# Kernel tuning notes

Hardware: AMD Instinct MI355X
Metric: run time of the kernel (lower is better)

The kernel has to match this reference:

```python
import jax, jax.numpy as jnp
import numpy as np
from functools import lru_cache


@lru_cache(maxsize=None)
def _mw_basis(L):
    """Fully-normalized associated Legendre basis on MW-style theta grid.

    Returns (Pfull, w):
      Pfull: (L, 2L-1, L) float32, Pfull[l, L-1+m, t] = Nbar_lm * P_l^m(cos theta_t)
             (zero for |m| > l), with Y_lm = Pfull * exp(i m phi).
      w:     (L,) float32 quadrature weights sin(theta)*dtheta*dphi.
    """
    t = np.arange(L)
    theta = np.pi * (2 * t + 1) / (2 * L - 1)  # MW theta samples
    ct, st = np.cos(theta), np.sin(theta)
    P = np.zeros((L, L, L))
    P[0, 0] = np.full(L, np.sqrt(1.0 / (4.0 * np.pi)))
    for m in range(1, L):
        P[m, m] = -np.sqrt((2.0 * m + 1.0) / (2.0 * m)) * st * P[m - 1, m - 1]
    for m in range(L - 1):
        P[m + 1, m] = np.sqrt(2.0 * m + 3.0) * ct * P[m, m]
    for m in range(L):
        for l in range(m + 2, L):
            a = np.sqrt((4.0 * l * l - 1.0) / (l * l - m * m))
            b = np.sqrt(((2.0 * l + 1.0) * (l - 1 - m) * (l - 1 + m)) / ((2.0 * l - 3.0) * (l * l - m * m)))
            P[l, m] = a * ct * P[l - 1, m] - b * P[l - 2, m]
    Pfull = np.zeros((L, 2 * L - 1, L), dtype=np.float32)
    for m in range(L):
        Pfull[:, L - 1 + m, :] = P[:, m, :]
        if m > 0:
            Pfull[:, L - 1 - m, :] = ((-1.0) ** m) * P[:, m, :]
    dang = 2.0 * np.pi / (2 * L - 1)  # theta and phi spacing
    w = (st * dang * dang).astype(np.float32)
    return jnp.asarray(Pfull), jnp.asarray(w)


def sht_forward(x):
    """x: (L, 2L-1, C) real -> flm: (L, 2L-1, C) complex, m indexed -(L-1)..(L-1)."""
    L = x.shape[0]
    P, w = _mw_basis(L)
    F = jnp.fft.fft(x.astype(jnp.complex64), axis=1)           # k = 0..2L-2
    F = jnp.concatenate([F[:, L:, :], F[:, :L, :]], axis=1)     # reorder to m = -(L-1)..L-1
    # flm = sum_t w_t Nbar P_l^m(theta_t) * Fm(theta_t)
    return jnp.einsum('lmt,tmc->lmc', P * w[None, None, :], F)


def sht_inverse(flm):
    """flm: (L, 2L-1, C) complex -> f: (L, 2L-1, C) complex on MW grid."""
    L = flm.shape[0]
    P, _ = _mw_basis(L)
    G = jnp.einsum('lmc,lmt->tmc', flm, P)                      # (theta, m, C)
    G = jnp.concatenate([G[:, L - 1:, :], G[:, :L - 1, :]], axis=1)  # m order -> fft k order
    return jnp.fft.ifft(G, axis=1) * (2 * L - 1)


def zero_pad_flm(flm, L_out):
    L_in = flm.shape[0]
    p = L_out - L_in
    return jnp.pad(flm, ((0, p), (p, p), (0, 0)))


L_IN = 256
L_FREQ = 128
L_OUT = 256
C_IN = 32
C_OUT = 32
T_DIM = 256


def setup_inputs() -> dict:
    key = jax.random.key(0)
    ks = jax.random.split(key, 8)
    return {
        'x': jax.random.normal(ks[0], (L_IN, 2 * L_IN - 1, C_IN), jnp.float32),
        't_emb': jax.random.normal(ks[1], (T_DIM,), jnp.float32),
        'weight_real': 0.02 * jax.random.normal(ks[2], (L_FREQ, C_IN, C_OUT), jnp.float32),
        'weight_imag': 0.02 * jax.random.normal(ks[3], (L_FREQ, C_IN, C_OUT), jnp.float32),
        'w_tr': jax.random.normal(ks[4], (T_DIM, L_FREQ), jnp.float32) / np.sqrt(T_DIM),
        'b_tr': jnp.zeros((L_FREQ,), jnp.float32),
        'w_ti': jax.random.normal(ks[5], (T_DIM, L_FREQ), jnp.float32) / np.sqrt(T_DIM),
        'b_ti': jnp.zeros((L_FREQ,), jnp.float32),
    }


def reference(x, t_emb, weight_real, weight_imag, w_tr, b_tr, w_ti, b_ti):
    # forward SHT over all channels at once
    flm = sht_forward(x)                                       # (L_in, 2L_in-1, C_in) complex64
    # bilinear resize of the spectrum to the used bandlimit (real/imag separately)
    tgt = (L_FREQ, 2 * L_FREQ - 1, flm.shape[2])
    flm = (jax.image.resize(jnp.real(flm), tgt, 'bilinear')
           + 1j * jax.image.resize(jnp.imag(flm), tgt, 'bilinear'))
    # time-modulated per-degree complex spectral weights
    t_cplx = (t_emb @ w_tr + b_tr) + 1j * (t_emb @ w_ti + b_ti)   # (L_freq,)
    weight = t_cplx[:, None, None] * (weight_real + 1j * weight_imag)  # (L_freq, C_in, C_out)
    flm = jnp.einsum('lmi,lio->lmo', flm, weight)
    # zero pad to output bandlimit and inverse SHT
    flm = zero_pad_flm(flm, L_OUT)                             # (L_out, 2L_out-1, C_out)
    x_out = jnp.real(sht_inverse(flm))
    return x_out
```

## Files before the change

kernel.cpp:

```cpp
#include <hip/hip_runtime.h>
#include <math.h>

#define PI_D 3.14159265358979323846

typedef short v8s __attribute__((ext_vector_type(8)));
typedef float v4f __attribute__((ext_vector_type(4)));

constexpr size_t OFF_PA   = 0;
constexpr size_t OFF_PT   = 8388608;
constexpr size_t OFF_SFRE = 12582912;
constexpr size_t OFF_SFIM = 14680064;
constexpr size_t OFF_FRE  = 16777216;
constexpr size_t OFF_FIM  = 18874368;
constexpr size_t OFF_CRE  = 20971520;
constexpr size_t OFF_CIM  = 22016000;
constexpr size_t OFF_AF   = 23060480;
constexpr size_t OFF_AI   = 23191552;
constexpr size_t OFF_WQ   = 23322624;
constexpr size_t OFF_TC   = 23322880;
constexpr size_t OFF_WLW  = 23323136;
constexpr size_t OFF_WLI  = 23323648;
constexpr size_t OFF_WMW  = 23324160;
constexpr size_t OFF_WMI  = 23325696;
constexpr size_t OFF_GRE  = OFF_FRE;
constexpr size_t OFF_GIM  = OFF_FIM;

__device__ __forceinline__ short f2bf(float f) {
  unsigned u = __float_as_uint(f);
  unsigned r = (u + 0x7FFFu + ((u >> 16) & 1u)) >> 16;
  return (short)r;
}


__device__ void phase_prep(const float* t_emb, const float* w_tr, const float* b_tr,
                           const float* w_ti, const float* b_ti, float* ws, int g0, int tid) {
  if (g0 < 2048) {
    int g = g0 * 256 + tid;
    bool inv = (g >= 262144);
    int gid = inv ? g - 262144 : g;
    int j = gid & 7, lane = (gid >> 3) & 63, ks = (gid >> 9) & 15, mt = gid >> 13;
    int m = mt * 16 + (lane & 15);
    int k = ks * 32 + ((lane >> 4) << 3) + j;
    float v = 0.f;
    if (!inv) {
      if (k < 511) {
        int mm = (m < 256) ? m : m - 256;
        int kk = (mm * k) % 511;
        float ang = (float)(2.0 * PI_D / 511.0) * (float)kk;
        float s, c; __sincosf(ang, &s, &c);
        v = (m < 256) ? c : -s;
      }
      ((short*)(ws + OFF_AF))[gid] = f2bf(v);
    } else {
      if (m < 511 && k < 510) {
        int jj = (k < 255) ? k : k - 255;
        int jm = jj - 127;
        int kk = ((jm * m) % 511 + 511) % 511;
        float ang = (float)(2.0 * PI_D / 511.0) * (float)kk;
        float s, c; __sincosf(ang, &s, &c);
        v = (k < 255) ? c : -s;
      }
      ((short*)(ws + OFF_AI))[gid] = f2bf(v);
    }
    return;
  }
  if (tid < 256) {
    double theta = PI_D * (2.0 * tid + 1.0) / 511.0;
    double dang = 2.0 * PI_D / 511.0;
    ws[OFF_WQ + tid] = (float)(sin(theta) * dang * dang);
  }
  {
    int h = tid >> 7, o = tid & 127;
    const float* W = h ? w_ti : w_tr;
    float s = h ? b_ti[o] : b_tr[o];
    for (int T = 0; T < 256; ++T) s += t_emb[T] * W[T * 128 + o];
    ws[OFF_TC + h * 128 + o] = s;
  }
  if (tid < 128) {
    double sf = 2.0 * tid + 0.5;
    double wv[4]; int iv[4]; double wsum = 0.0;
    for (int a = 0; a < 4; ++a) {
      int t = 2 * tid - 1 + a;
      double r = 1.0 - fabs(sf - (double)t) * 0.5;
      bool valid = (t >= 0 && t < 256 && r > 0.0);
      wv[a] = valid ? r : 0.0; iv[a] = valid ? t : 0;
      wsum += wv[a];
    }
    for (int a = 0; a < 4; ++a) {
      ws[OFF_WLW + tid * 4 + a] = (float)(wv[a] / wsum);
      ((int*)(ws + OFF_WLI))[tid * 4 + a] = iv[a];
    }
  }
  if (tid < 255) {
    double inv2 = 511.0 / 255.0;
    double sf = (tid + 0.5) * inv2 - 0.5;
    int t0 = (int)floor(sf) - 2;
    double wv[6]; int iv[6]; double wsum = 0.0;
    for (int b = 0; b < 6; ++b) {
      int t = t0 + b;
      double r = 1.0 - fabs(sf - (double)t) * (255.0 / 511.0);
      bool valid = (t >= 0 && t < 511 && r > 0.0);
      wv[b] = valid ? r : 0.0; iv[b] = valid ? t : 0;
      wsum += wv[b];
    }
    for (int b = 0; b < 6; ++b) {
      ws[OFF_WMW + tid * 6 + b] = (float)(wv[b] / wsum);
      ((int*)(ws + OFF_WMI))[tid * 6 + b] = iv[b];
    }
  }
}

__device__ void phase_legendre(float* ws, char* smem, int m, int t) {
  double* cA = (double*)smem;
  double* cB = cA + 256;
  double* cS = cB + 256;
  short* tile = (short*)(smem + 6144);
  short* tileT = (short*)(smem + 6144 + 8960);
  {
    int l = t;
    if (l >= 1) cS[l] = -sqrt((2.0 * l + 1.0) / (2.0 * l));
    if (l >= m + 2) {
      double ll = l, mm = m;
      double den = ll * ll - mm * mm;
      cA[l] = sqrt((4.0 * ll * ll - 1.0) / den);
      cB[l] = sqrt((2.0 * ll + 1.0) * (ll - 1.0 - mm) * (ll - 1.0 + mm) /
                   ((2.0 * ll - 3.0) * den));
    }
  }
  __syncthreads();
  bool wantPT = (m < 128);
  short* PAp = (short*)(ws + OFF_PA) + (size_t)m * 65536;
  short* PTp = (short*)(ws + OFF_PT) + (size_t)m * 65536;
  double theta = PI_D * (2.0 * t + 1.0) / 511.0;
  double ct = cos(theta), st = sin(theta);
  double p0 = sqrt(1.0 / (4.0 * PI_D));
  for (int k = 1; k <= m; ++k) p0 *= cS[k] * st;
  double pm1 = 0.0, pcur = 0.0;
  for (int lt = 0; lt < 16; ++lt) {
    for (int li = 0; li < 16; ++li) {
      int l = lt * 16 + li;
      float v;
      if (l < m) v = 0.f;
      else if (l == m) { pcur = p0; v = (float)pcur; }
      else if (l == m + 1) { pm1 = pcur; pcur = sqrt(2.0 * m + 3.0) * ct * pm1; v = (float)pcur; }
      else { double p2 = cA[l] * ct * pcur - cB[l] * pm1; pm1 = pcur; pcur = p2; v = (float)p2; }
      short bv = f2bf(v);
      tile[li * 280 + t] = bv;
      if (wantPT) tileT[t * 34 + li] = bv;
    }
    __syncthreads();
#pragma unroll
    for (int pass = 0; pass < 2; ++pass) {
      int ch = pass * 256 + t;
      int li = ch & 15, T0 = ch >> 4;
      size_t dst = (size_t)lt * 4096 + (size_t)(T0 >> 2) * 512 + (size_t)((T0 & 3) * 16 + li) * 8;
      *(v8s*)(PAp + dst) = *(const v8s*)(tile + li * 280 + T0 * 8);
    }
    if (wantPT) {
#pragma unroll
      for (int pass = 0; pass < 2; ++pass) {
        int ch = pass * 256 + t;
        int tt = ch >> 1, li0 = (ch & 1) * 8;
        size_t dst = (size_t)(tt >> 4) * 4096 + (size_t)(lt >> 1) * 512 +
                     (size_t)(((lt & 1) * 2 + (li0 >> 3)) * 16 + (tt & 15)) * 8;
        const int* src = (const int*)(tileT + tt * 34 + li0);
        int* d = (int*)(PTp + dst);
        d[0] = src[0]; d[1] = src[1]; d[2] = src[2]; d[3] = src[3];
      }
    }
    __syncthreads();
  }
}

__device__ void phase_gemm_f(const float* x, float* ws, short* lds, int uid, int tid) {
  int nt = uid & 1, mh = (uid >> 1) & 1, t = uid >> 2;
  int wave = tid >> 6, lane = tid & 63;
  const v8s* A = (const v8s*)(ws + OFF_AF);
  float wq = ws[OFF_WQ + t];
  const float* row = x + (size_t)t * 511 * 32 + nt * 16;
  int cl = lane & 15, quad = lane >> 4;
  int mtB = mh * 16 + wave * 4;
  int ck = tid >> 4, cc = tid & 15;
  v4f acc[4];
#pragma unroll
  for (int i = 0; i < 4; ++i) acc[i] = (v4f){0.f, 0.f, 0.f, 0.f};
  v8s a_cur[4], a_nxt[4];
#pragma unroll
  for (int i = 0; i < 4; ++i) a_cur[i] = A[(size_t)((mtB + i) * 16 + 0) * 64 + lane];
  {
    float p0 = wq * row[(size_t)ck * 32 + cc];
    float p1 = wq * row[(size_t)(ck + 16) * 32 + cc];
    lds[cc * 40 + ck] = f2bf(p0);
    lds[cc * 40 + ck + 16] = f2bf(p1);
  }
  __syncthreads();
  for (int ks = 0; ks < 16; ++ks) {
    float n0 = 0.f, n1 = 0.f;
    if (ks < 15) {
      int ph0 = (ks + 1) * 32 + ck, ph1 = ph0 + 16;
      n0 = (ph0 < 511) ? wq * row[(size_t)ph0 * 32 + cc] : 0.f;
      n1 = (ph1 < 511) ? wq * row[(size_t)ph1 * 32 + cc] : 0.f;
#pragma unroll
      for (int i = 0; i < 4; ++i)
        a_nxt[i] = A[(size_t)((mtB + i) * 16 + ks + 1) * 64 + lane];
    }
    v8s b = *(const v8s*)(lds + (ks & 1) * 640 + cl * 40 + quad * 8);
#pragma unroll
    for (int i = 0; i < 4; ++i)
      acc[i] = __builtin_amdgcn_mfma_f32_16x16x32_bf16(a_cur[i], b, acc[i], 0, 0, 0);
    if (ks < 15) {
      short* nb = lds + ((ks + 1) & 1) * 640;
      nb[cc * 40 + ck] = f2bf(n0);
      nb[cc * 40 + ck + 16] = f2bf(n1);
#pragma unroll
      for (int i = 0; i < 4; ++i) a_cur[i] = a_nxt[i];
      __syncthreads();
    }
  }
  int cn = nt * 16 + cl;
#pragma unroll
  for (int i = 0; i < 4; ++i) {
    int mt = mtB + i;
#pragma unroll
    for (int r = 0; r < 4; ++r) {
      int mp = mt * 16 + quad * 4 + r;
      float v = acc[i][r];
      if (mp < 256) ws[OFF_FRE + ((size_t)mp * 256 + t) * 32 + cn] = v;
      else          ws[OFF_FIM + ((size_t)(mp - 256) * 256 + t) * 32 + cn] = v;
    }
  }
}

__device__ void phase_legfwd(float* ws, short* lds, int uid, int tid) {
  int m = uid >> 2, q = uid & 3;
  int lane = tid & 63;
  int cl = lane & 15, quad = lane >> 4;
  if (q * 64 + 63 < m) {
    int mt = q * 4 + (tid >> 6);
#pragma unroll
    for (int n = 0; n < 4; ++n) {
      int cp = n * 16 + cl;
      float* dst = ws + ((cp >= 32) ? OFF_SFIM : OFF_SFRE) + (size_t)m * 8192 + (cp & 31);
#pragma unroll
      for (int r = 0; r < 4; ++r) {
        int l = mt * 16 + quad * 4 + r;
        dst[(size_t)l * 32] = 0.f;
      }
    }
    return;
  }
  int mt = q * 4 + (tid >> 6);
  bool sk = (mt * 16 + 15) < m;
  const v8s* A = (const v8s*)(ws + OFF_PA) + (size_t)m * 8192;
  int half = (tid >> 5) & 1, c = tid & 31, tb = tid >> 6;
  const float* srcb = ws + (half ? OFF_FIM : OFF_FRE) + (size_t)m * 8192 + c;
  short* myrow = lds;
  int ldsw = (half * 32 + c) * 40 + tb;
  v4f acc[4];
#pragma unroll
  for (int n = 0; n < 4; ++n) acc[n] = (v4f){0.f, 0.f, 0.f, 0.f};
  v8s a_cur = A[(size_t)mt * 512 + lane];
  v8s a_nxt;
  {
    float pv[8];
#pragma unroll
    for (int pass = 0; pass < 8; ++pass)
      pv[pass] = srcb[(size_t)(pass * 4 + tb) * 32];
#pragma unroll
    for (int pass = 0; pass < 8; ++pass)
      myrow[ldsw + pass * 4] = f2bf(pv[pass]);
  }
  __syncthreads();
  for (int ks = 0; ks < 8; ++ks) {
    float pn[8];
    if (ks < 7) {
#pragma unroll
      for (int pass = 0; pass < 8; ++pass)
        pn[pass] = srcb[(size_t)((ks + 1) * 32 + pass * 4 + tb) * 32];
      a_nxt = A[(size_t)mt * 512 + (ks + 1) * 64 + lane];
    }
    const short* cur = lds + (ks & 1) * 2560;
    if (!sk) {
#pragma unroll
      for (int n = 0; n < 4; ++n) {
        v8s b = *(const v8s*)(cur + (n * 16 + cl) * 40 + quad * 8);
        acc[n] = __builtin_amdgcn_mfma_f32_16x16x32_bf16(a_cur, b, acc[n], 0, 0, 0);
      }
    }
    if (ks < 7) {
      short* nb = lds + ((ks + 1) & 1) * 2560;
#pragma unroll
      for (int pass = 0; pass < 8; ++pass)
        nb[ldsw + pass * 4] = f2bf(pn[pass]);
      a_cur = a_nxt;
      __syncthreads();
    }
  }
#pragma unroll
  for (int n = 0; n < 4; ++n) {
    int cp = n * 16 + cl;
    float* dst = ws + ((cp >= 32) ? OFF_SFIM : OFF_SFRE) + (size_t)m * 8192 + (cp & 31);
#pragma unroll
    for (int r = 0; r < 4; ++r) {
      int l = mt * 16 + quad * 4 + r;
      dst[(size_t)l * 32] = sk ? 0.f : acc[n][r];
    }
  }
}

__device__ void phase_conv(const float* w_real, const float* w_imag, float* ws, char* smem,
                           int uid, int tid) {
  int l = uid >> 3, jq8 = uid & 7;
  int jl = tid >> 5, o = tid & 31;
  float* wr = (float*)smem;
  float* wi = wr + 32 * 36;
  float* fr = wi + 32 * 36;
  float* fi = fr + 8 * 32;
  {
    int oo = tid >> 3, i4 = (tid & 7) * 4;
    float tcr = ws[OFF_TC + l], tci = ws[OFF_TC + 128 + l];
#pragma unroll
    for (int q = 0; q < 4; ++q) {
      int i = i4 + q;
      float a = w_real[(size_t)l * 1024 + i * 32 + oo];
      float b = w_imag[(size_t)l * 1024 + i * 32 + oo];
      wr[oo * 36 + i] = tcr * a - tci * b;
      wi[oo * 36 + i] = tcr * b + tci * a;
    }
  }
  const float* SFRE = ws + OFF_SFRE;
  const float* SFIM = ws + OFF_SFIM;
  const float* WMW = ws + OFF_WMW;
  const int* WMI = (const int*)(ws + OFF_WMI);
  float wl[4]; int liv[4];
#pragma unroll
  for (int a = 0; a < 4; ++a) {
    wl[a] = ws[OFF_WLW + l * 4 + a];
    liv[a] = ((const int*)(ws + OFF_WLI))[l * 4 + a];
  }
  for (int ji = 0; ji < 4; ++ji) {
    int j = jq8 * 32 + ji * 8 + jl;
    int jp = (j < 255) ? j : 254;
    float accr = 0.f, acci = 0.f;
    for (int b = 0; b < 6; ++b) {
      float wm = WMW[jp * 6 + b];
      int jm = WMI[jp * 6 + b];
      bool mneg = (jm < 255);
      int mm = mneg ? (255 - jm) : (jm - 255);
      float fre_f = (mneg && (mm & 1)) ? -1.f : 1.f;
      float fim_f = mneg ? -fre_f : 1.f;
#pragma unroll
      for (int a = 0; a < 4; ++a) {
        float w = wm * wl[a];
        size_t base = ((size_t)mm * 256 + liv[a]) * 32 + o;
        accr = fmaf(w * fre_f, SFRE[base], accr);
        acci = fmaf(w * fim_f, SFIM[base], acci);
      }
    }
    __syncthreads();
    fr[jl * 32 + o] = accr;
    fi[jl * 32 + o] = acci;
    __syncthreads();
    float sr = 0.f, si = 0.f;
#pragma unroll
    for (int i0 = 0; i0 < 32; i0 += 4) {
      float4 f_r = *(const float4*)(fr + jl * 32 + i0);
      float4 f_i = *(const float4*)(fi + jl * 32 + i0);
      float4 w_r = *(const float4*)(wr + o * 36 + i0);
      float4 w_i = *(const float4*)(wi + o * 36 + i0);
      sr += f_r.x * w_r.x - f_i.x * w_i.x;  si += f_r.x * w_i.x + f_i.x * w_r.x;
      sr += f_r.y * w_r.y - f_i.y * w_i.y;  si += f_r.y * w_i.y + f_i.y * w_r.y;
      sr += f_r.z * w_r.z - f_i.z * w_i.z;  si += f_r.z * w_i.z + f_i.z * w_r.z;
      sr += f_r.w * w_r.w - f_i.w * w_i.w;  si += f_r.w * w_i.w + f_i.w * w_r.w;
    }
    if (j < 255) {
      float s = (j < 127 && ((127 - j) & 1)) ? -1.f : 1.f;
      ws[OFF_CRE + ((size_t)j * 128 + l) * 32 + o] = s * sr;
      ws[OFF_CIM + ((size_t)j * 128 + l) * 32 + o] = s * si;
    }
  }
}

__device__ void phase_linv(float* ws, int uid, int tid) {
  int j = uid >> 2;
  int d = j - 127; int mm = (d < 0) ? -d : d;
  int mt = (uid & 3) * 4 + (tid >> 6), lane = tid & 63;
  const v8s* A = (const v8s*)(ws + OFF_PT) + (size_t)mm * 8192;
  int cl = lane & 15, lB = (lane >> 4) << 3;
  int quad = lane >> 4;
  v4f acc[4];
#pragma unroll
  for (int n = 0; n < 4; ++n) acc[n] = (v4f){0.f, 0.f, 0.f, 0.f};
  int ks0 = mm >> 5;
  const float* Cb[4];
#pragma unroll
  for (int n = 0; n < 4; ++n) {
    int cp = n * 16 + cl;
    Cb[n] = ws + (cp < 32 ? OFF_CRE : OFF_CIM) + ((size_t)j * 128 + lB) * 32 + (cp & 31);
  }
  float bv[4][8];
  v8s a_cur = A[(size_t)mt * 512 + ks0 * 64 + lane];
#pragma unroll
  for (int n = 0; n < 4; ++n)
#pragma unroll
    for (int j8 = 0; j8 < 8; ++j8) bv[n][j8] = Cb[n][(size_t)(ks0 * 32 + j8) * 32];
  for (int ks = ks0; ks < 4; ++ks) {
    float bn[4][8];
    v8s a_nxt;
    if (ks < 3) {
#pragma unroll
      for (int n = 0; n < 4; ++n)
#pragma unroll
        for (int j8 = 0; j8 < 8; ++j8) bn[n][j8] = Cb[n][(size_t)((ks + 1) * 32 + j8) * 32];
      a_nxt = A[(size_t)mt * 512 + (ks + 1) * 64 + lane];
    }
#pragma unroll
    for (int n = 0; n < 4; ++n) {
      v8s b;
#pragma unroll
      for (int j8 = 0; j8 < 8; ++j8) b[j8] = f2bf(bv[n][j8]);
      acc[n] = __builtin_amdgcn_mfma_f32_16x16x32_bf16(a_cur, b, acc[n], 0, 0, 0);
    }
    if (ks < 3) {
#pragma unroll
      for (int n = 0; n < 4; ++n)
#pragma unroll
        for (int j8 = 0; j8 < 8; ++j8) bv[n][j8] = bn[n][j8];
      a_cur = a_nxt;
    }
  }
#pragma unroll
  for (int n = 0; n < 4; ++n) {
    int cp = n * 16 + cl;
    float* dst = ws + ((cp >= 32) ? OFF_GIM : OFF_GRE) + (size_t)(cp & 31);
#pragma unroll
    for (int r = 0; r < 4; ++r) {
      int t = mt * 16 + quad * 4 + r;
      dst[((size_t)t * 255 + j) * 32] = acc[n][r];
    }
  }
}

__device__ void phase_gemm_i(const float* ws, float* out, short* lds, int uid, int tid) {
  int nt = uid & 1, mh = (uid >> 1) & 1, t = uid >> 2;
  int wave = tid >> 6, lane = tid & 63;
  const v8s* A = (const v8s*)(ws + OFF_AI);
  const float* GRE = ws + OFF_GRE;
  const float* GIM = ws + OFF_GIM;
  int cl = lane & 15, quad = lane >> 4;
  int mtB = mh * 16 + wave * 4;
  int cn = nt * 16 + cl;
  int ck = tid >> 4, cc = tid & 15;
  int ccg = nt * 16 + cc;
  v4f acc[4];
#pragma unroll
  for (int i = 0; i < 4; ++i) acc[i] = (v4f){0.f, 0.f, 0.f, 0.f};
  v8s a_cur[4], a_nxt[4];
#pragma unroll
  for (int i = 0; i < 4; ++i) a_cur[i] = A[(size_t)((mtB + i) * 16 + 0) * 64 + lane];
  {
    float p0 = GRE[((size_t)t * 255 + ck) * 32 + ccg];
    float p1 = GRE[((size_t)t * 255 + ck + 16) * 32 + ccg];
    lds[cc * 40 + ck] = f2bf(p0);
    lds[cc * 40 + ck + 16] = f2bf(p1);
  }
  __syncthreads();
  for (int ks = 0; ks < 16; ++ks) {
    float n0 = 0.f, n1 = 0.f;
    if (ks < 15) {
      int k0 = (ks + 1) * 32 + ck, k1 = k0 + 16;
      if (k0 < 255)      n0 = GRE[((size_t)t * 255 + k0) * 32 + ccg];
      else if (k0 < 510) n0 = GIM[((size_t)t * 255 + (k0 - 255)) * 32 + ccg];
      if (k1 < 255)      n1 = GRE[((size_t)t * 255 + k1) * 32 + ccg];
      else if (k1 < 510) n1 = GIM[((size_t)t * 255 + (k1 - 255)) * 32 + ccg];
#pragma unroll
      for (int i = 0; i < 4; ++i)
        a_nxt[i] = A[(size_t)((mtB + i) * 16 + ks + 1) * 64 + lane];
    }
    v8s b = *(const v8s*)(lds + (ks & 1) * 640 + cl * 40 + quad * 8);
#pragma unroll
    for (int i = 0; i < 4; ++i)
      acc[i] = __builtin_amdgcn_mfma_f32_16x16x32_bf16(a_cur[i], b, acc[i], 0, 0, 0);
    if (ks < 15) {
      short* nb = lds + ((ks + 1) & 1) * 640;
      nb[cc * 40 + ck] = f2bf(n0);
      nb[cc * 40 + ck + 16] = f2bf(n1);
#pragma unroll
      for (int i = 0; i < 4; ++i) a_cur[i] = a_nxt[i];
      __syncthreads();
    }
  }
#pragma unroll
  for (int i = 0; i < 4; ++i) {
    int mt = mtB + i;
#pragma unroll
    for (int r = 0; r < 4; ++r) {
      int phi = mt * 16 + quad * 4 + r;
      if (phi < 511) out[((size_t)t * 511 + phi) * 32 + cn] = acc[i][r];
    }
  }
}

__global__ __launch_bounds__(256) void k_prepleg(const float* t_emb, const float* w_tr,
                                                 const float* b_tr, const float* w_ti,
                                                 const float* b_ti, float* ws) {
  __shared__ __align__(16) char smem[32768];
  int bid = blockIdx.x;
  if (bid < 256) phase_legendre(ws, smem, bid, threadIdx.x);
  else phase_prep(t_emb, w_tr, b_tr, w_ti, b_ti, ws, bid - 256, threadIdx.x);
}
__global__ __launch_bounds__(256) void kw_gemm_f(const float* x, float* ws) {
  __shared__ __align__(16) short lds[2 * 640];
  phase_gemm_f(x, ws, lds, blockIdx.x, threadIdx.x);
}
__global__ __launch_bounds__(256) void kw_legfwd(float* ws) {
  __shared__ __align__(16) short lds[2 * 2560];
  phase_legfwd(ws, lds, blockIdx.x, threadIdx.x);
}
__global__ __launch_bounds__(256) void kw_conv(const float* w_real, const float* w_imag, float* ws) {
  __shared__ __align__(16) char smem[11264];
  phase_conv(w_real, w_imag, ws, smem, blockIdx.x, threadIdx.x);
}
__global__ __launch_bounds__(256) void kw_linv(float* ws) {
  phase_linv(ws, blockIdx.x, threadIdx.x);
}
__global__ __launch_bounds__(256) void kw_gemm_i(const float* ws, float* out) {
  __shared__ __align__(16) short lds[2 * 640];
  phase_gemm_i(ws, out, lds, blockIdx.x, threadIdx.x);
}

extern "C" void kernel_launch(void* const* d_in, const int* in_sizes, int n_in,
                              void* d_out, int out_size, void* d_ws, size_t ws_size,
                              hipStream_t stream) {
  const float* x = (const float*)d_in[0];
  const float* t_emb = (const float*)d_in[1];
  const float* w_real = (const float*)d_in[2];
  const float* w_imag = (const float*)d_in[3];
  const float* w_tr = (const float*)d_in[4];
  const float* b_tr = (const float*)d_in[5];
  const float* w_ti = (const float*)d_in[6];
  const float* b_ti = (const float*)d_in[7];
  float* ws = (float*)d_ws;
  float* out = (float*)d_out;
  (void)in_sizes; (void)n_in; (void)out_size; (void)ws_size;

  hipLaunchKernelGGL(k_prepleg, dim3(2305), dim3(256), 0, stream,
                     t_emb, w_tr, b_tr, w_ti, b_ti, ws);
  hipLaunchKernelGGL(kw_gemm_f, dim3(1024), dim3(256), 0, stream, x, ws);
  hipLaunchKernelGGL(kw_legfwd, dim3(1024), dim3(256), 0, stream, ws);
  hipLaunchKernelGGL(kw_conv, dim3(1024), dim3(256), 0, stream, w_real, w_imag, ws);
  hipLaunchKernelGGL(kw_linv, dim3(1020), dim3(256), 0, stream, ws);
  hipLaunchKernelGGL(kw_gemm_i, dim3(1024), dim3(256), 0, stream, ws, out);
}
```

Before: 188.3 us.

## Stage full B operand in LDS upfront and skip zero Legendre tile stores

Three GEMM phases (forward DFT GEMM, forward Legendre, inverse DFT GEMM) now load the whole B operand into LDS once, using packed 8-wide bf16 stores, and no longer double-buffer it. This removes the per-iteration barriers and the interleaved global loads inside the k-loop. The forward Legendre phase also skips A-tile loads for fully-zero m tiles. The Legendre table builder skips writing tiles that lie entirely below l=m, assuming those regions are never read or are already zero. The cost is a much larger LDS footprint per block (about 16–33KB), which may lower occupancy, and the global loads are no longer overlapped with the MFMAs.

```diff
diff --git a/kernel.cpp b/kernel.cpp
--- a/kernel.cpp
+++ b/kernel.cpp
@@ -149,14 +149,16 @@
       if (wantPT) tileT[t * 34 + li] = bv;
     }
     __syncthreads();
-#pragma unroll
-    for (int pass = 0; pass < 2; ++pass) {
-      int ch = pass * 256 + t;
-      int li = ch & 15, T0 = ch >> 4;
-      size_t dst = (size_t)lt * 4096 + (size_t)(T0 >> 2) * 512 + (size_t)((T0 & 3) * 16 + li) * 8;
-      *(v8s*)(PAp + dst) = *(const v8s*)(tile + li * 280 + T0 * 8);
-    }
-    if (wantPT) {
+    if (lt * 16 + 15 >= m) {
+#pragma unroll
+      for (int pass = 0; pass < 2; ++pass) {
+        int ch = pass * 256 + t;
+        int li = ch & 15, T0 = ch >> 4;
+        size_t dst = (size_t)lt * 4096 + (size_t)(T0 >> 2) * 512 + (size_t)((T0 & 3) * 16 + li) * 8;
+        *(v8s*)(PAp + dst) = *(const v8s*)(tile + li * 280 + T0 * 8);
+      }
+    }
+    if (wantPT && ((lt >> 1) >= (m >> 5))) {
 #pragma unroll
       for (int pass = 0; pass < 2; ++pass) {
         int ch = pass * 256 + t;
@@ -180,41 +182,43 @@
   const float* row = x + (size_t)t * 511 * 32 + nt * 16;
   int cl = lane & 15, quad = lane >> 4;
   int mtB = mh * 16 + wave * 4;
-  int ck = tid >> 4, cc = tid & 15;
+  {
+    int c = tid & 15, kc = tid >> 4;
+#pragma unroll
+    for (int i = 0; i < 4; ++i) {
+      int k0 = (kc + 16 * i) * 8;
+      float pv[8];
+#pragma unroll
+      for (int j = 0; j < 8; ++j) {
+        int k = k0 + j;
+        pv[j] = (k < 511) ? wq * row[(size_t)k * 32 + c] : 0.f;
+      }
+      v8s tmp;
+#pragma unroll
+      for (int j = 0; j < 8; ++j) tmp[j] = f2bf(pv[j]);
+      *(v8s*)(lds + c * 520 + k0) = tmp;
+    }
+  }
   v4f acc[4];
 #pragma unroll
   for (int i = 0; i < 4; ++i) acc[i] = (v4f){0.f, 0.f, 0.f, 0.f};
   v8s a_cur[4], a_nxt[4];
 #pragma unroll
   for (int i = 0; i < 4; ++i) a_cur[i] = A[(size_t)((mtB + i) * 16 + 0) * 64 + lane];
-  {
-    float p0 = wq * row[(size_t)ck * 32 + cc];
-    float p1 = wq * row[(size_t)(ck + 16) * 32 + cc];
-    lds[cc * 40 + ck] = f2bf(p0);
-    lds[cc * 40 + ck + 16] = f2bf(p1);
-  }
   __syncthreads();
   for (int ks = 0; ks < 16; ++ks) {
-    float n0 = 0.f, n1 = 0.f;
     if (ks < 15) {
-      int ph0 = (ks + 1) * 32 + ck, ph1 = ph0 + 16;
-      n0 = (ph0 < 511) ? wq * row[(size_t)ph0 * 32 + cc] : 0.f;
-      n1 = (ph1 < 511) ? wq * row[(size_t)ph1 * 32 + cc] : 0.f;
 #pragma unroll
       for (int i = 0; i < 4; ++i)
         a_nxt[i] = A[(size_t)((mtB + i) * 16 + ks + 1) * 64 + lane];
     }
-    v8s b = *(const v8s*)(lds + (ks & 1) * 640 + cl * 40 + quad * 8);
+    v8s b = *(const v8s*)(lds + cl * 520 + ks * 32 + quad * 8);
 #pragma unroll
     for (int i = 0; i < 4; ++i)
       acc[i] = __builtin_amdgcn_mfma_f32_16x16x32_bf16(a_cur[i], b, acc[i], 0, 0, 0);
     if (ks < 15) {
-      short* nb = lds + ((ks + 1) & 1) * 640;
-      nb[cc * 40 + ck] = f2bf(n0);
-      nb[cc * 40 + ck + 16] = f2bf(n1);
 #pragma unroll
       for (int i = 0; i < 4; ++i) a_cur[i] = a_nxt[i];
-      __syncthreads();
     }
   }
   int cn = nt * 16 + cl;
@@ -252,48 +256,37 @@
   int mt = q * 4 + (tid >> 6);
   bool sk = (mt * 16 + 15) < m;
   const v8s* A = (const v8s*)(ws + OFF_PA) + (size_t)m * 8192;
-  int half = (tid >> 5) & 1, c = tid & 31, tb = tid >> 6;
-  const float* srcb = ws + (half ? OFF_FIM : OFF_FRE) + (size_t)m * 8192 + c;
-  short* myrow = lds;
-  int ldsw = (half * 32 + c) * 40 + tb;
+  {
+    int half = (tid >> 5) & 1, c = tid & 31, tb = tid >> 6;
+    const float* srcb = ws + (half ? OFF_FIM : OFF_FRE) + (size_t)m * 8192 + c;
+    int ldsrow = (half * 32 + c) * 264;
+#pragma unroll
+    for (int p = 0; p < 8; ++p) {
+      int t0 = (p * 4 + tb) * 8;
+      float pv[8];
+#pragma unroll
+      for (int j = 0; j < 8; ++j) pv[j] = srcb[(size_t)(t0 + j) * 32];
+      v8s tmp;
+#pragma unroll
+      for (int j = 0; j < 8; ++j) tmp[j] = f2bf(pv[j]);
+      *(v8s*)(lds + ldsrow + t0) = tmp;
+    }
+  }
   v4f acc[4];
 #pragma unroll
   for (int n = 0; n < 4; ++n) acc[n] = (v4f){0.f, 0.f, 0.f, 0.f};
-  v8s a_cur = A[(size_t)mt * 512 + lane];
-  v8s a_nxt;
-  {
-    float pv[8];
-#pragma unroll
-    for (int pass = 0; pass < 8; ++pass)
-      pv[pass] = srcb[(size_t)(pass * 4 + tb) * 32];
-#pragma unroll
-    for (int pass = 0; pass < 8; ++pass)
-      myrow[ldsw + pass * 4] = f2bf(pv[pass]);
-  }
+  v8s a_cur, a_nxt;
+  if (!sk) a_cur = A[(size_t)mt * 512 + lane];
   __syncthreads();
   for (int ks = 0; ks < 8; ++ks) {
-    float pn[8];
-    if (ks < 7) {
-#pragma unroll
-      for (int pass = 0; pass < 8; ++pass)
-        pn[pass] = srcb[(size_t)((ks + 1) * 32 + pass * 4 + tb) * 32];
-      a_nxt = A[(size_t)mt * 512 + (ks + 1) * 64 + lane];
-    }
-    const short* cur = lds + (ks & 1) * 2560;
+    if (!sk && ks < 7) a_nxt = A[(size_t)mt * 512 + (ks + 1) * 64 + lane];
     if (!sk) {
 #pragma unroll
       for (int n = 0; n < 4; ++n) {
-        v8s b = *(const v8s*)(cur + (n * 16 + cl) * 40 + quad * 8);
+        v8s b = *(const v8s*)(lds + (n * 16 + cl) * 264 + ks * 32 + quad * 8);
         acc[n] = __builtin_amdgcn_mfma_f32_16x16x32_bf16(a_cur, b, acc[n], 0, 0, 0);
       }
-    }
-    if (ks < 7) {
-      short* nb = lds + ((ks + 1) & 1) * 2560;
-#pragma unroll
-      for (int pass = 0; pass < 8; ++pass)
-        nb[ldsw + pass * 4] = f2bf(pn[pass]);
-      a_cur = a_nxt;
-      __syncthreads();
+      if (ks < 7) a_cur = a_nxt;
     }
   }
 #pragma unroll
@@ -450,44 +443,47 @@
   int cl = lane & 15, quad = lane >> 4;
   int mtB = mh * 16 + wave * 4;
   int cn = nt * 16 + cl;
-  int ck = tid >> 4, cc = tid & 15;
-  int ccg = nt * 16 + cc;
+  {
+    int c = tid & 15, kc = tid >> 4;
+    int ccg = nt * 16 + c;
+#pragma unroll
+    for (int i = 0; i < 4; ++i) {
+      int k0 = (kc + 16 * i) * 8;
+      float pv[8];
+#pragma unroll
+      for (int j = 0; j < 8; ++j) {
+        int k = k0 + j;
+        float v = 0.f;
+        if (k < 255)      v = GRE[((size_t)t * 255 + k) * 32 + ccg];
+        else if (k < 510) v = GIM[((size_t)t * 255 + (k - 255)) * 32 + ccg];
+        pv[j] = v;
+      }
+      v8s tmp;
+#pragma unroll
+      for (int j = 0; j < 8; ++j) tmp[j] = f2bf(pv[j]);
+      *(v8s*)(lds + c * 520 + k0) = tmp;
+    }
+  }
   v4f acc[4];
 #pragma unroll
   for (int i = 0; i < 4; ++i) acc[i] = (v4f){0.f, 0.f, 0.f, 0.f};
   v8s a_cur[4], a_nxt[4];
 #pragma unroll
   for (int i = 0; i < 4; ++i) a_cur[i] = A[(size_t)((mtB + i) * 16 + 0) * 64 + lane];
-  {
-    float p0 = GRE[((size_t)t * 255 + ck) * 32 + ccg];
-    float p1 = GRE[((size_t)t * 255 + ck + 16) * 32 + ccg];
-    lds[cc * 40 + ck] = f2bf(p0);
-    lds[cc * 40 + ck + 16] = f2bf(p1);
-  }
   __syncthreads();
   for (int ks = 0; ks < 16; ++ks) {
-    float n0 = 0.f, n1 = 0.f;
     if (ks < 15) {
-      int k0 = (ks + 1) * 32 + ck, k1 = k0 + 16;
-      if (k0 < 255)      n0 = GRE[((size_t)t * 255 + k0) * 32 + ccg];
-      else if (k0 < 510) n0 = GIM[((size_t)t * 255 + (k0 - 255)) * 32 + ccg];
-      if (k1 < 255)      n1 = GRE[((size_t)t * 255 + k1) * 32 + ccg];
-      else if (k1 < 510) n1 = GIM[((size_t)t * 255 + (k1 - 255)) * 32 + ccg];
 #pragma unroll
       for (int i = 0; i < 4; ++i)
         a_nxt[i] = A[(size_t)((mtB + i) * 16 + ks + 1) * 64 + lane];
     }
-    v8s b = *(const v8s*)(lds + (ks & 1) * 640 + cl * 40 + quad * 8);
+    v8s b = *(const v8s*)(lds + cl * 520 + ks * 32 + quad * 8);
 #pragma unroll
     for (int i = 0; i < 4; ++i)
       acc[i] = __builtin_amdgcn_mfma_f32_16x16x32_bf16(a_cur[i], b, acc[i], 0, 0, 0);
     if (ks < 15) {
-      short* nb = lds + ((ks + 1) & 1) * 640;
-      nb[cc * 40 + ck] = f2bf(n0);
-      nb[cc * 40 + ck + 16] = f2bf(n1);
 #pragma unroll
       for (int i = 0; i < 4; ++i) a_cur[i] = a_nxt[i];
-      __syncthreads();
     }
   }
 #pragma unroll
@@ -510,11 +506,11 @@
   else phase_prep(t_emb, w_tr, b_tr, w_ti, b_ti, ws, bid - 256, threadIdx.x);
 }
 __global__ __launch_bounds__(256) void kw_gemm_f(const float* x, float* ws) {
-  __shared__ __align__(16) short lds[2 * 640];
+  __shared__ __align__(16) short lds[16 * 520];
   phase_gemm_f(x, ws, lds, blockIdx.x, threadIdx.x);
 }
 __global__ __launch_bounds__(256) void kw_legfwd(float* ws) {
-  __shared__ __align__(16) short lds[2 * 2560];
+  __shared__ __align__(16) short lds[64 * 264];
   phase_legfwd(ws, lds, blockIdx.x, threadIdx.x);
 }
 __global__ __launch_bounds__(256) void kw_conv(const float* w_real, const float* w_imag, float* ws) {
@@ -525,7 +521,7 @@
   phase_linv(ws, blockIdx.x, threadIdx.x);
 }
 __global__ __launch_bounds__(256) void kw_gemm_i(const float* ws, float* out) {
-  __shared__ __align__(16) short lds[2 * 640];
+  __shared__ __align__(16) short lds[16 * 520];
   phase_gemm_i(ws, out, lds, blockIdx.x, threadIdx.x);
 }
 
```

New measurement: 197.5 us. 1.05x slower.
